# Optimization experiments

Measured on AMD Instinct MI355X. Metric: run time of the kernel, lower is better.

## Reference

```python
import jax, jax.numpy as jnp
import numpy as np
from jax import lax

K = 3        # kernel_size
PAD = 1      # padding
STRIDE = 1   # stride


def conv2d(x, w, stride, pad):
    return lax.conv_general_dilated(
        x, w, (stride, stride), [(pad, pad), (pad, pad)],
        dimension_numbers=('NCHW', 'OIHW', 'NCHW'))


def setup_inputs() -> dict:
    key = jax.random.key(0)
    ks = jax.random.split(key, 8)
    B, Ci, Cc, H, W = 8, 64, 64, 128, 128
    K2 = K * K
    return {
        'x_img': jax.random.normal(ks[0], (B, Ci, H, W), jnp.float32),
        'x_cont': jax.random.normal(ks[1], (B, Cc, H, W), jnp.float32),
        'w_fuse': jax.random.normal(ks[2], (Ci, Ci + Cc, 1, 1), jnp.float32) * 0.05,
        'w_off': jax.random.normal(ks[3], (2 * K2, Ci, K, K), jnp.float32) * 0.01,
        'b_off': jax.random.normal(ks[4], (2 * K2,), jnp.float32) * 0.1,
        'w_mod': jax.random.normal(ks[5], (K2, Ci, K, K), jnp.float32) * 0.01,
        'b_mod': jax.random.normal(ks[6], (K2,), jnp.float32) * 0.1,
        'w_reg': jax.random.normal(ks[7], (Ci, Ci, K, K), jnp.float32) * 0.05,
    }


def _bilinear_sample(img, py, px):
    # Zero padding outside the image (per-corner validity, matches torchvision).
    C, Hin, Win = img.shape
    flat = img.reshape(C, -1)
    y0 = jnp.floor(py)
    x0 = jnp.floor(px)

    def gather(yy, xx):
        valid = (yy >= 0) & (yy <= Hin - 1) & (xx >= 0) & (xx <= Win - 1)
        yc = jnp.clip(yy, 0, Hin - 1).astype(jnp.int32)
        xc = jnp.clip(xx, 0, Win - 1).astype(jnp.int32)
        return flat[:, yc * Win + xc] * valid[None].astype(img.dtype)

    wy1 = py - y0; wy0 = 1.0 - wy1
    wx1 = px - x0; wx0 = 1.0 - wx1
    return (gather(y0, x0) * (wy0 * wx0)[None]
            + gather(y0, x0 + 1.0) * (wy0 * wx1)[None]
            + gather(y0 + 1.0, x0) * (wy1 * wx0)[None]
            + gather(y0 + 1.0, x0 + 1.0) * (wy1 * wx1)[None])


def reference(x_img, x_cont, w_fuse, w_off, b_off, w_mod, b_mod, w_reg):
    # 1x1 fuse of image features with control factor
    x = conv2d(jnp.concatenate([x_img, x_cont], axis=1), w_fuse, 1, 0)
    # offset / modulator branches
    off = conv2d(x, w_off, STRIDE, PAD) + b_off[None, :, None, None]
    mod = 2.0 * jax.nn.sigmoid(conv2d(x, w_mod, STRIDE, PAD) + b_mod[None, :, None, None])
    B, C, Hin, Win = x.shape
    K2 = K * K
    Hout, Wout = off.shape[2], off.shape[3]
    # torchvision layout: channel 2k = dy, 2k+1 = dx for kernel pos k = i*K + j
    off = off.reshape(B, K2, 2, Hout, Wout)
    dy, dx = off[:, :, 0], off[:, :, 1]
    ky = (jnp.arange(K2) // K).astype(x.dtype)
    kx = (jnp.arange(K2) % K).astype(x.dtype)
    base_y = (jnp.arange(Hout) * STRIDE - PAD).astype(x.dtype)
    base_x = (jnp.arange(Wout) * STRIDE - PAD).astype(x.dtype)
    py = dy + base_y[None, None, :, None] + ky[None, :, None, None]  # [B,K2,H,W]
    px = dx + base_x[None, None, None, :] + kx[None, :, None, None]
    sampled = jax.vmap(_bilinear_sample)(x, py, px)          # [B,C,K2,H,W]
    sampled = sampled * mod[:, None]                          # modulation
    out = jnp.einsum('oik,bikhw->bohw', w_reg.reshape(C, C, K2), sampled)
    return out
```

## Files before the change

kernel.cpp:

```cpp
#include <hip/hip_runtime.h>
#include <math.h>

#define B_   8
#define C_   64
#define H_   128
#define W_   128
#define HW_  16384
#define K2_  9

typedef float f32x4 __attribute__((ext_vector_type(4)));
typedef short bf16x8 __attribute__((ext_vector_type(8)));
typedef unsigned short u16x4 __attribute__((ext_vector_type(4)));
typedef unsigned int u32x4 __attribute__((ext_vector_type(4)));

#define WS_WRP  8192
#define WS_WRP2 26624
#define WS_XT   45056
#define WS_OM   8433664

static __device__ __forceinline__ unsigned short f2bf(float x) {
    unsigned int u = __float_as_uint(x);
    unsigned int r = (u + 0x7fffu + ((u >> 16) & 1u)) >> 16;
    return (unsigned short)r;
}
static __device__ __forceinline__ float bf2f(unsigned short u) {
    return __uint_as_float(((unsigned int)u) << 16);
}
static __device__ __forceinline__ unsigned int cvt_pk_bf16(float lo, float hi) {
    unsigned int r;
    asm("v_cvt_pk_bf16_f32 %0, %1, %2" : "=v"(r) : "v"(lo), "v"(hi));
    return r;
}

__global__ __launch_bounds__(256) void k_fuse(const float* __restrict__ xi,
                                              const float* __restrict__ xc,
                                              const float* __restrict__ wf,
                                              const float* __restrict__ wreg,
                                              const float* __restrict__ wOff,
                                              const float* __restrict__ wMod,
                                              unsigned short* __restrict__ xtb,
                                              unsigned short* __restrict__ wrP,
                                              unsigned short* __restrict__ wrP2) {
    __shared__ unsigned short sA[1024 * 8];
    const int t = threadIdx.x;
    const int lane = t & 63;
    const int wv = t >> 6;
    const int b = blockIdx.x & 7;
    const int yh = blockIdx.x >> 3;
    const int y = yh >> 1;
    const int h = yh & 1;

    if (blockIdx.x < 18) {
        const int idx = blockIdx.x * 256 + t;
        if (idx < 4608) {
            int ln = idx & 63, mt = (idx >> 6) & 3, kc = (idx >> 8) & 1, tap = idx >> 9;
            int o = mt * 16 + (ln & 15);
            int ibase = kc * 32 + (ln >> 4) * 8;
#pragma unroll
            for (int j = 0; j < 8; ++j)
                wrP[idx * 8 + j] = f2bf(wreg[(o * 64 + ibase + j) * 9 + tap]);
        }
        if (idx < 2304) {
            int ln = idx & 63, mt = (idx >> 6) & 1, kc = idx >> 7;
            int m = mt * 16 + (ln & 15);
            int gkb = kc * 32 + (ln >> 4) * 8;
#pragma unroll
            for (int j = 0; j < 8; ++j) {
                int gk = gkb + j, tap = gk >> 6, ci = gk & 63;
                float v = 0.f;
                if (m < 18)      v = wOff[(m * 64 + ci) * 9 + tap];
                else if (m < 27) v = wMod[((m - 18) * 64 + ci) * 9 + tap];
                wrP2[idx * 8 + j] = f2bf(v);
            }
        }
    }

#pragma unroll
    for (int r = 0; r < 4; ++r) {
        const int c = t + 256 * r;
        const int f = c >> 6;
        const int ln = c & 63;
        const int mt = f & 3, kc = f >> 2;
        const int m = mt * 16 + (ln & 15);
        const int kb = kc * 32 + (ln >> 4) * 8;
        const float* s = wf + m * 128 + kb;
        unsigned short us[8];
#pragma unroll
        for (int j = 0; j < 8; ++j) us[j] = f2bf(s[j]);
        *(bf16x8*)&sA[c * 8] = *(const bf16x8*)us;
    }
    __syncthreads();

    const int n15 = lane & 15;
    const int q4 = lane >> 4;
    const int px = h * 64 + wv * 16 + n15;
    const size_t poff = (size_t)y * W_ + px;

    f32x4 acc[4];
#pragma unroll
    for (int mt = 0; mt < 4; ++mt) acc[mt] = (f32x4){0.f, 0.f, 0.f, 0.f};

#pragma unroll
    for (int kc = 0; kc < 4; ++kc) {
        const float* src = (kc < 2)
            ? (xi + ((size_t)(b * 64 + kc * 32 + q4 * 8)) * HW_ + poff)
            : (xc + ((size_t)(b * 64 + (kc - 2) * 32 + q4 * 8)) * HW_ + poff);
        unsigned short us[8];
#pragma unroll
        for (int j = 0; j < 8; ++j) us[j] = f2bf(src[(size_t)j * HW_]);
        const bf16x8 bf = *(const bf16x8*)us;
#pragma unroll
        for (int mt = 0; mt < 4; ++mt) {
            const bf16x8 a = *(const bf16x8*)&sA[((kc * 4 + mt) * 64 + lane) * 8];
            acc[mt] = __builtin_amdgcn_mfma_f32_16x16x32_bf16(a, bf, acc[mt], 0, 0, 0);
        }
    }

#pragma unroll
    for (int mt = 0; mt < 4; ++mt) {
        u16x4 o4;
        o4.x = f2bf(acc[mt][0]); o4.y = f2bf(acc[mt][1]);
        o4.z = f2bf(acc[mt][2]); o4.w = f2bf(acc[mt][3]);
        *(u16x4*)&xtb[((size_t)b * HW_ + poff) * 64 + mt * 16 + q4 * 4] = o4;
    }
}

__global__ __launch_bounds__(256) void k_offmod(const unsigned short* __restrict__ xtb,
                                                const unsigned short* __restrict__ wrP2,
                                                const float* __restrict__ bOff,
                                                const float* __restrict__ bMod,
                                                float* __restrict__ om) {
    __shared__ unsigned short sB[3 * 66 * 72];
    const int t = threadIdx.x;
    const int lane = t & 63;
    const int wv = t >> 6;
    const int b = blockIdx.x & 7;
    const int yh = blockIdx.x >> 3;
    const int y = yh >> 1;
    const int h = yh & 1;

    for (int idx = t; idx < 3 * 66 * 8; idx += 256) {
        const int c8 = idx & 7;
        const int pp = (idx >> 3) % 66;
        const int row = (idx >> 3) / 66;
        const int gx = h * 64 + pp - 1;
        const int gy = y + row - 1;
        bf16x8 v = {0, 0, 0, 0, 0, 0, 0, 0};
        if (gx >= 0 && gx < W_ && gy >= 0 && gy < H_)
            v = *(const bf16x8*)&xtb[(((size_t)(b * H_ + gy)) * W_ + gx) * 64 + c8 * 8];
        *(bf16x8*)&sB[(row * 66 + pp) * 72 + c8 * 8] = v;
    }
    __syncthreads();

    const int n15 = lane & 15;
    const int q4 = lane >> 4;

    f32x4 acc[2];
    acc[0] = (f32x4){0.f, 0.f, 0.f, 0.f};
    acc[1] = (f32x4){0.f, 0.f, 0.f, 0.f};

#pragma unroll
    for (int kc = 0; kc < 18; ++kc) {
        const int gkb = kc * 32 + q4 * 8;
        const int tap = gkb >> 6;
        const int ci = gkb & 63;
        const int row = tap / 3, kx = tap % 3;
        const bf16x8 bf = *(const bf16x8*)&sB[(row * 66 + (wv * 16 + n15 + kx)) * 72 + ci];
        const bf16x8 a0 = *(const bf16x8*)(wrP2 + (((size_t)(kc * 2 + 0) * 64 + lane) * 8));
        const bf16x8 a1 = *(const bf16x8*)(wrP2 + (((size_t)(kc * 2 + 1) * 64 + lane) * 8));
        acc[0] = __builtin_amdgcn_mfma_f32_16x16x32_bf16(a0, bf, acc[0], 0, 0, 0);
        acc[1] = __builtin_amdgcn_mfma_f32_16x16x32_bf16(a1, bf, acc[1], 0, 0, 0);
    }

    const int px = h * 64 + wv * 16 + n15;
    const size_t rec = ((size_t)(b * H_ + y)) * 28 * 128;
#pragma unroll
    for (int mt = 0; mt < 2; ++mt)
#pragma unroll
        for (int r = 0; r < 4; ++r) {
            const int o = mt * 16 + q4 * 4 + r;
            if (o < 18) {
                const int c = (o >> 1) + ((o & 1) ? 9 : 0);
                om[rec + c * 128 + px] = acc[mt][r] + bOff[o];
            } else if (o < 27) {
                const float z = acc[mt][r] + bMod[o - 18];
                om[rec + (18 + (o - 18)) * 128 + px] = 2.f / (1.f + __expf(-z));
            }
        }
}

__global__ __launch_bounds__(256) void k_deform(const unsigned short* __restrict__ xtb,
                                                const float* __restrict__ om,
                                                const unsigned short* __restrict__ wrP,
                                                float* __restrict__ out) {
    const int t = threadIdx.x;
    const int lane = t & 63;
    const int wv = t >> 6;
    const int b = blockIdx.x & 7;
    const int yh = blockIdx.x >> 3;
    const int y = yh >> 1;
    const int h = yh & 1;

    const char* xbB = (const char*)(xtb + (size_t)b * HW_ * 64);
    const float* omr = om + ((size_t)(b * H_ + y)) * 28 * 128;

    const int n15 = lane & 15;
    const int q4 = lane >> 4;
    const int px = h * 64 + wv * 16 + n15;

    f32x4 acc[4];
#pragma unroll
    for (int mt = 0; mt < 4; ++mt) acc[mt] = (f32x4){0.f, 0.f, 0.f, 0.f};

    for (int k = 0; k < 9; ++k) {
        const int ky = k / 3 - 1, kx = k % 3 - 1;

        const float dy  = omr[k * 128 + px];
        const float dxv = omr[(9 + k) * 128 + px];
        const float m   = omr[(18 + k) * 128 + px];
        const float py  = (float)(y + ky) + dy;
        const float pxe = (float)(px + kx) + dxv;
        const float y0f = floorf(py), x0f = floorf(pxe);
        const int y0i = (int)y0f, x0i = (int)x0f;
        const float wy1 = py - y0f, wx1 = pxe - x0f;
        const float wy0 = 1.f - wy1, wx0 = 1.f - wx1;

        int   offs[4];
        float wts[4];
#pragma unroll
        for (int c = 0; c < 4; ++c) {
            const int cy = c >> 1, cx = c & 1;
            const int yy = y0i + cy;
            const int xx = x0i + cx;
            const bool ok = (yy >= 0) && (yy < H_) && (xx >= 0) && (xx < W_);
            const int yc = min(max(yy, 0), H_ - 1);
            const int xc = min(max(xx, 0), W_ - 1);
            offs[c] = (yc * W_ + xc) * 128 + q4 * 16;
            wts[c] = ok ? (cy ? wy1 : wy0) * (cx ? wx1 : wx0) * m : 0.f;
        }

        const u32x4 g00 = *(const u32x4*)(xbB + offs[0]);
        const u32x4 g01 = *(const u32x4*)(xbB + offs[1]);
        const u32x4 g02 = *(const u32x4*)(xbB + offs[2]);
        const u32x4 g03 = *(const u32x4*)(xbB + offs[3]);
        const u32x4 g10 = *(const u32x4*)(xbB + offs[0] + 64);
        const u32x4 g11 = *(const u32x4*)(xbB + offs[1] + 64);
        const u32x4 g12 = *(const u32x4*)(xbB + offs[2] + 64);
        const u32x4 g13 = *(const u32x4*)(xbB + offs[3] + 64);

        const float w0 = wts[0], w1 = wts[1], w2 = wts[2], w3 = wts[3];

#pragma unroll
        for (int kc = 0; kc < 2; ++kc) {
            const u32x4 c0 = kc ? g10 : g00;
            const u32x4 c1 = kc ? g11 : g01;
            const u32x4 c2 = kc ? g12 : g02;
            const u32x4 c3 = kc ? g13 : g03;
            unsigned int outw[4];
#pragma unroll
            for (int d = 0; d < 4; ++d) {
                const float lo = __uint_as_float(c0[d] << 16) * w0
                               + __uint_as_float(c1[d] << 16) * w1
                               + __uint_as_float(c2[d] << 16) * w2
                               + __uint_as_float(c3[d] << 16) * w3;
                const float hi = __uint_as_float(c0[d] & 0xffff0000u) * w0
                               + __uint_as_float(c1[d] & 0xffff0000u) * w1
                               + __uint_as_float(c2[d] & 0xffff0000u) * w2
                               + __uint_as_float(c3[d] & 0xffff0000u) * w3;
                outw[d] = cvt_pk_bf16(lo, hi);
            }
            const bf16x8 bfB = *(const bf16x8*)outw;
#pragma unroll
            for (int mt = 0; mt < 4; ++mt) {
                const bf16x8 a = *(const bf16x8*)(wrP +
                    ((((size_t)((k * 2 + kc) * 4 + mt)) * 64 + lane) * 8));
                acc[mt] = __builtin_amdgcn_mfma_f32_16x16x32_bf16(a, bfB, acc[mt], 0, 0, 0);
            }
        }
    }

#pragma unroll
    for (int mt = 0; mt < 4; ++mt)
#pragma unroll
        for (int r = 0; r < 4; ++r) {
            const int o = mt * 16 + q4 * 4 + r;
            out[(((size_t)(b * 64 + o)) * H_ + y) * W_ + px] = acc[mt][r];
        }
}

extern "C" void kernel_launch(void* const* d_in, const int* in_sizes, int n_in,
                              void* d_out, int out_size, void* d_ws, size_t ws_size,
                              hipStream_t stream) {
    const float* x_img  = (const float*)d_in[0];
    const float* x_cont = (const float*)d_in[1];
    const float* w_fuse = (const float*)d_in[2];
    const float* w_off  = (const float*)d_in[3];
    const float* b_off  = (const float*)d_in[4];
    const float* w_mod  = (const float*)d_in[5];
    const float* b_mod  = (const float*)d_in[6];
    const float* w_reg  = (const float*)d_in[7];
    float* out = (float*)d_out;

    float* ws  = (float*)d_ws;
    unsigned short* wrP  = (unsigned short*)(ws + WS_WRP);
    unsigned short* wrP2 = (unsigned short*)(ws + WS_WRP2);
    unsigned short* xtb  = (unsigned short*)(ws + WS_XT);
    float* om  = ws + WS_OM;

    k_fuse<<<B_ * H_ * 2, 256, 0, stream>>>(x_img, x_cont, w_fuse, w_reg, w_off,
                                            w_mod, xtb, wrP, wrP2);
    k_offmod<<<B_ * H_ * 2, 256, 0, stream>>>(xtb, wrP2, b_off, b_mod, om);
    k_deform<<<B_ * H_ * 2, 256, 0, stream>>>(xtb, om, wrP, out);
}
```

Measured before the change: 222.9 us.

## Software-pipeline deformable gathers with double-buffered registers and preloaded offsets

Preloads all 27 offset and modulator values per pixel into registers up front. The 9-tap loop is fully unrolled and double-buffered, so the bilinear corner gathers for tap k+1 are issued before the blend and MFMA work for tap k. This is meant to hide global gather latency behind compute. It raises register pressure (two sets of eight 128-bit vectors plus 27 floats), which could reduce occupancy.

Measured after the change: 222.3 us. Within noise of the previous version (-0.2%).

```diff
diff --git a/kernel.cpp b/kernel.cpp
--- a/kernel.cpp
+++ b/kernel.cpp
@@ -189,6 +189,67 @@
         }
 }
 
+
+#define STAGE(K, S) do {                                                      \
+    const float dy_  = omv[(K)];                                              \
+    const float dxv_ = omv[9 + (K)];                                          \
+    const float m_   = omv[18 + (K)];                                         \
+    const float py_  = (float)(y + ((K) / 3 - 1)) + dy_;                      \
+    const float pxe_ = (float)(px + ((K) % 3 - 1)) + dxv_;                    \
+    const float y0f_ = floorf(py_), x0f_ = floorf(pxe_);                      \
+    const int y0i_ = (int)y0f_, x0i_ = (int)x0f_;                             \
+    const float wy1_ = py_ - y0f_, wx1_ = pxe_ - x0f_;                        \
+    const float wy0_ = 1.f - wy1_, wx0_ = 1.f - wx1_;                         \
+    _Pragma("unroll")                                                         \
+    for (int c_ = 0; c_ < 4; ++c_) {                                          \
+        const int cy_ = c_ >> 1, cx_ = c_ & 1;                                \
+        const int yy_ = y0i_ + cy_;                                           \
+        const int xx_ = x0i_ + cx_;                                           \
+        const bool ok_ = (yy_ >= 0) && (yy_ < H_) && (xx_ >= 0) && (xx_ < W_);\
+        const int yc_ = min(max(yy_, 0), H_ - 1);                             \
+        const int xc_ = min(max(xx_, 0), W_ - 1);                             \
+        const int off_ = (yc_ * W_ + xc_) * 128 + q4 * 16;                    \
+        wts[S][c_] = ok_ ? (cy_ ? wy1_ : wy0_) * (cx_ ? wx1_ : wx0_) * m_     \
+                         : 0.f;                                               \
+        g[S][c_]     = *(const u32x4*)(xbB + off_);                           \
+        g[S][4 + c_] = *(const u32x4*)(xbB + off_ + 64);                      \
+    }                                                                         \
+} while (0)
+
+#define BLEND(K, S) do {                                                      \
+    const float w0_ = wts[S][0], w1_ = wts[S][1];                             \
+    const float w2_ = wts[S][2], w3_ = wts[S][3];                             \
+    _Pragma("unroll")                                                         \
+    for (int kc_ = 0; kc_ < 2; ++kc_) {                                       \
+        unsigned int outw_[4];                                                \
+        _Pragma("unroll")                                                     \
+        for (int d_ = 0; d_ < 4; ++d_) {                                      \
+            const unsigned int a_ = g[S][kc_ * 4 + 0][d_];                    \
+            const unsigned int b_ = g[S][kc_ * 4 + 1][d_];                    \
+            const unsigned int c_ = g[S][kc_ * 4 + 2][d_];                    \
+            const unsigned int e_ = g[S][kc_ * 4 + 3][d_];                    \
+            const float lo_ = __uint_as_float(a_ << 16) * w0_                 \
+                            + __uint_as_float(b_ << 16) * w1_                 \
+                            + __uint_as_float(c_ << 16) * w2_                 \
+                            + __uint_as_float(e_ << 16) * w3_;                \
+            const float hi_ = __uint_as_float(a_ & 0xffff0000u) * w0_         \
+                            + __uint_as_float(b_ & 0xffff0000u) * w1_         \
+                            + __uint_as_float(c_ & 0xffff0000u) * w2_         \
+                            + __uint_as_float(e_ & 0xffff0000u) * w3_;        \
+            outw_[d_] = cvt_pk_bf16(lo_, hi_);                                \
+        }                                                                     \
+        const bf16x8 bfB_ = *(const bf16x8*)outw_;                            \
+        _Pragma("unroll")                                                     \
+        for (int mt_ = 0; mt_ < 4; ++mt_) {                                   \
+            const bf16x8 a2_ = *(const bf16x8*)(wrP +                         \
+                ((((size_t)(((K) * 2 + kc_) * 4 + mt_)) * 64 + lane) * 8));   \
+            acc[mt_] = __builtin_amdgcn_mfma_f32_16x16x32_bf16(a2_, bfB_,     \
+                                                               acc[mt_],     \
+                                                               0, 0, 0);      \
+        }                                                                     \
+    }                                                                         \
+} while (0)
+
 __global__ __launch_bounds__(256) void k_deform(const unsigned short* __restrict__ xtb,
                                                 const float* __restrict__ om,
                                                 const unsigned short* __restrict__ wrP,
@@ -208,75 +269,26 @@
     const int q4 = lane >> 4;
     const int px = h * 64 + wv * 16 + n15;
 
+    float omv[27];
+#pragma unroll
+    for (int i = 0; i < 27; ++i) omv[i] = omr[i * 128 + px];
+
     f32x4 acc[4];
 #pragma unroll
     for (int mt = 0; mt < 4; ++mt) acc[mt] = (f32x4){0.f, 0.f, 0.f, 0.f};
 
+    u32x4 g[2][8];
+    float wts[2][4];
+
+    STAGE(0, 0);
+#pragma unroll
     for (int k = 0; k < 9; ++k) {
-        const int ky = k / 3 - 1, kx = k % 3 - 1;
-
-        const float dy  = omr[k * 128 + px];
-        const float dxv = omr[(9 + k) * 128 + px];
-        const float m   = omr[(18 + k) * 128 + px];
-        const float py  = (float)(y + ky) + dy;
-        const float pxe = (float)(px + kx) + dxv;
-        const float y0f = floorf(py), x0f = floorf(pxe);
-        const int y0i = (int)y0f, x0i = (int)x0f;
-        const float wy1 = py - y0f, wx1 = pxe - x0f;
-        const float wy0 = 1.f - wy1, wx0 = 1.f - wx1;
-
-        int   offs[4];
-        float wts[4];
-#pragma unroll
-        for (int c = 0; c < 4; ++c) {
-            const int cy = c >> 1, cx = c & 1;
-            const int yy = y0i + cy;
-            const int xx = x0i + cx;
-            const bool ok = (yy >= 0) && (yy < H_) && (xx >= 0) && (xx < W_);
-            const int yc = min(max(yy, 0), H_ - 1);
-            const int xc = min(max(xx, 0), W_ - 1);
-            offs[c] = (yc * W_ + xc) * 128 + q4 * 16;
-            wts[c] = ok ? (cy ? wy1 : wy0) * (cx ? wx1 : wx0) * m : 0.f;
-        }
-
-        const u32x4 g00 = *(const u32x4*)(xbB + offs[0]);
-        const u32x4 g01 = *(const u32x4*)(xbB + offs[1]);
-        const u32x4 g02 = *(const u32x4*)(xbB + offs[2]);
-        const u32x4 g03 = *(const u32x4*)(xbB + offs[3]);
-        const u32x4 g10 = *(const u32x4*)(xbB + offs[0] + 64);
-        const u32x4 g11 = *(const u32x4*)(xbB + offs[1] + 64);
-        const u32x4 g12 = *(const u32x4*)(xbB + offs[2] + 64);
-        const u32x4 g13 = *(const u32x4*)(xbB + offs[3] + 64);
-
-        const float w0 = wts[0], w1 = wts[1], w2 = wts[2], w3 = wts[3];
-
-#pragma unroll
-        for (int kc = 0; kc < 2; ++kc) {
-            const u32x4 c0 = kc ? g10 : g00;
-            const u32x4 c1 = kc ? g11 : g01;
-            const u32x4 c2 = kc ? g12 : g02;
-            const u32x4 c3 = kc ? g13 : g03;
-            unsigned int outw[4];
-#pragma unroll
-            for (int d = 0; d < 4; ++d) {
-                const float lo = __uint_as_float(c0[d] << 16) * w0
-                               + __uint_as_float(c1[d] << 16) * w1
-                               + __uint_as_float(c2[d] << 16) * w2
-                               + __uint_as_float(c3[d] << 16) * w3;
-                const float hi = __uint_as_float(c0[d] & 0xffff0000u) * w0
-                               + __uint_as_float(c1[d] & 0xffff0000u) * w1
-                               + __uint_as_float(c2[d] & 0xffff0000u) * w2
-                               + __uint_as_float(c3[d] & 0xffff0000u) * w3;
-                outw[d] = cvt_pk_bf16(lo, hi);
-            }
-            const bf16x8 bfB = *(const bf16x8*)outw;
-#pragma unroll
-            for (int mt = 0; mt < 4; ++mt) {
-                const bf16x8 a = *(const bf16x8*)(wrP +
-                    ((((size_t)((k * 2 + kc) * 4 + mt)) * 64 + lane) * 8));
-                acc[mt] = __builtin_amdgcn_mfma_f32_16x16x32_bf16(a, bfB, acc[mt], 0, 0, 0);
-            }
-        }
+        if (k < 8) {
+            if ((k & 1) == 0) STAGE(k + 1, 1);
+            else              STAGE(k + 1, 0);
+        }
+        if ((k & 1) == 0) BLEND(k, 0);
+        else              BLEND(k, 1);
     }
 
 #pragma unroll
```

## Stage local 5x68 input window in LDS for deformable bilinear gathers

Applied to the files above, without the earlier changes.

The deform kernel now cooperatively loads a 5-row by 68-column bf16 window of the fused features around the block's output row into shared memory. Each bilinear corner reads from LDS when it falls inside the window and otherwise falls back to a global load (a dummy address when inside). All 27 offset and modulator values are also preloaded into registers before the tap loop. The aim is to replace scattered global gathers with LDS reads. The cost is a staging pass, a barrier, extra LDS use that lowers occupancy, and a global load that is still issued for every corner even when it is not needed.

Measured after the change: 194.5 us. 12.7% less time.

```diff
diff --git a/kernel.cpp b/kernel.cpp
--- a/kernel.cpp
+++ b/kernel.cpp
@@ -29,6 +29,14 @@
 static __device__ __forceinline__ unsigned int cvt_pk_bf16(float lo, float hi) {
     unsigned int r;
     asm("v_cvt_pk_bf16_f32 %0, %1, %2" : "=v"(r) : "v"(lo), "v"(hi));
+    return r;
+}
+static __device__ __forceinline__ u32x4 sel4(bool c, u32x4 a, u32x4 b) {
+    u32x4 r;
+    r[0] = c ? a[0] : b[0];
+    r[1] = c ? a[1] : b[1];
+    r[2] = c ? a[2] : b[2];
+    r[3] = c ? a[3] : b[3];
     return r;
 }
 
@@ -193,6 +201,7 @@
                                                 const float* __restrict__ om,
                                                 const unsigned short* __restrict__ wrP,
                                                 float* __restrict__ out) {
+    __shared__ __align__(16) unsigned short sW[5 * 68 * 72];
     const int t = threadIdx.x;
     const int lane = t & 63;
     const int wv = t >> 6;
@@ -200,6 +209,21 @@
     const int yh = blockIdx.x >> 3;
     const int y = yh >> 1;
     const int h = yh & 1;
+    const int wx0 = h * 64 - 2;
+    const int ylo = y - 2;
+
+    for (int i = t; i < 2720; i += 256) {
+        const int c8 = i & 7;
+        const int p  = (i >> 3) % 68;
+        const int r  = (i >> 3) / 68;
+        const int gx = wx0 + p;
+        const int gy = ylo + r;
+        bf16x8 v = {0, 0, 0, 0, 0, 0, 0, 0};
+        if (gx >= 0 && gx < W_ && gy >= 0 && gy < H_)
+            v = *(const bf16x8*)&xtb[(((size_t)(b * H_ + gy)) * W_ + gx) * 64 + c8 * 8];
+        *(bf16x8*)&sW[(r * 68 + p) * 72 + c8 * 8] = v;
+    }
+    __syncthreads();
 
     const char* xbB = (const char*)(xtb + (size_t)b * HW_ * 64);
     const float* omr = om + ((size_t)(b * H_ + y)) * 28 * 128;
@@ -208,24 +232,27 @@
     const int q4 = lane >> 4;
     const int px = h * 64 + wv * 16 + n15;
 
+    float omv[27];
+#pragma unroll
+    for (int i = 0; i < 27; ++i) omv[i] = omr[i * 128 + px];
+
     f32x4 acc[4];
 #pragma unroll
     for (int mt = 0; mt < 4; ++mt) acc[mt] = (f32x4){0.f, 0.f, 0.f, 0.f};
 
     for (int k = 0; k < 9; ++k) {
         const int ky = k / 3 - 1, kx = k % 3 - 1;
-
-        const float dy  = omr[k * 128 + px];
-        const float dxv = omr[(9 + k) * 128 + px];
-        const float m   = omr[(18 + k) * 128 + px];
+        const float dy  = omv[k];
+        const float dxv = omv[9 + k];
+        const float m   = omv[18 + k];
         const float py  = (float)(y + ky) + dy;
         const float pxe = (float)(px + kx) + dxv;
         const float y0f = floorf(py), x0f = floorf(pxe);
         const int y0i = (int)y0f, x0i = (int)x0f;
         const float wy1 = py - y0f, wx1 = pxe - x0f;
-        const float wy0 = 1.f - wy1, wx0 = 1.f - wx1;
-
-        int   offs[4];
+        const float wy0 = 1.f - wy1, wx0f = 1.f - wx1;
+
+        u32x4 gv[8];
         float wts[4];
 #pragma unroll
         for (int c = 0; c < 4; ++c) {
@@ -233,40 +260,46 @@
             const int yy = y0i + cy;
             const int xx = x0i + cx;
             const bool ok = (yy >= 0) && (yy < H_) && (xx >= 0) && (xx < W_);
+            wts[c] = ok ? (cy ? wy1 : wy0) * (cx ? wx1 : wx0f) * m : 0.f;
+            const bool inw = (yy >= ylo) && (yy <= ylo + 4)
+                          && (xx >= wx0) && (xx < wx0 + 68);
+            int wr = yy - ylo; wr = min(max(wr, 0), 4);
+            int wc = xx - wx0; wc = min(max(wc, 0), 67);
+            const int lsW = (wr * 68 + wc) * 72 + q4 * 8;
+            const bf16x8 l0 = *(const bf16x8*)&sW[lsW];
+            const bf16x8 l1 = *(const bf16x8*)&sW[lsW + 32];
             const int yc = min(max(yy, 0), H_ - 1);
             const int xc = min(max(xx, 0), W_ - 1);
-            offs[c] = (yc * W_ + xc) * 128 + q4 * 16;
-            wts[c] = ok ? (cy ? wy1 : wy0) * (cx ? wx1 : wx0) * m : 0.f;
-        }
-
-        const u32x4 g00 = *(const u32x4*)(xbB + offs[0]);
-        const u32x4 g01 = *(const u32x4*)(xbB + offs[1]);
-        const u32x4 g02 = *(const u32x4*)(xbB + offs[2]);
-        const u32x4 g03 = *(const u32x4*)(xbB + offs[3]);
-        const u32x4 g10 = *(const u32x4*)(xbB + offs[0] + 64);
-        const u32x4 g11 = *(const u32x4*)(xbB + offs[1] + 64);
-        const u32x4 g12 = *(const u32x4*)(xbB + offs[2] + 64);
-        const u32x4 g13 = *(const u32x4*)(xbB + offs[3] + 64);
+            const int off = inw ? (q4 * 16) : ((yc * W_ + xc) * 128 + q4 * 16);
+            const bf16x8 g0 = *(const bf16x8*)(xbB + off);
+            const bf16x8 g1 = *(const bf16x8*)(xbB + off + 64);
+            u32x4 lu0, lu1, gu0, gu1;
+            __builtin_memcpy(&lu0, &l0, 16);
+            __builtin_memcpy(&lu1, &l1, 16);
+            __builtin_memcpy(&gu0, &g0, 16);
+            __builtin_memcpy(&gu1, &g1, 16);
+            gv[c]     = sel4(inw, lu0, gu0);
+            gv[4 + c] = sel4(inw, lu1, gu1);
+        }
 
         const float w0 = wts[0], w1 = wts[1], w2 = wts[2], w3 = wts[3];
-
 #pragma unroll
         for (int kc = 0; kc < 2; ++kc) {
-            const u32x4 c0 = kc ? g10 : g00;
-            const u32x4 c1 = kc ? g11 : g01;
-            const u32x4 c2 = kc ? g12 : g02;
-            const u32x4 c3 = kc ? g13 : g03;
             unsigned int outw[4];
 #pragma unroll
             for (int d = 0; d < 4; ++d) {
-                const float lo = __uint_as_float(c0[d] << 16) * w0
-                               + __uint_as_float(c1[d] << 16) * w1
-                               + __uint_as_float(c2[d] << 16) * w2
-                               + __uint_as_float(c3[d] << 16) * w3;
-                const float hi = __uint_as_float(c0[d] & 0xffff0000u) * w0
-                               + __uint_as_float(c1[d] & 0xffff0000u) * w1
-                               + __uint_as_float(c2[d] & 0xffff0000u) * w2
-                               + __uint_as_float(c3[d] & 0xffff0000u) * w3;
+                const unsigned int av = gv[kc * 4 + 0][d];
+                const unsigned int bv = gv[kc * 4 + 1][d];
+                const unsigned int cv = gv[kc * 4 + 2][d];
+                const unsigned int ev = gv[kc * 4 + 3][d];
+                const float lo = __uint_as_float(av << 16) * w0
+                               + __uint_as_float(bv << 16) * w1
+                               + __uint_as_float(cv << 16) * w2
+                               + __uint_as_float(ev << 16) * w3;
+                const float hi = __uint_as_float(av & 0xffff0000u) * w0
+                               + __uint_as_float(bv & 0xffff0000u) * w1
+                               + __uint_as_float(cv & 0xffff0000u) * w2
+                               + __uint_as_float(ev & 0xffff0000u) * w3;
                 outw[d] = cvt_pk_bf16(lo, hi);
             }
             const bf16x8 bfB = *(const bf16x8*)outw;
```
